# Kernel optimization log

Measured on AMD Instinct MI355X. Metric: run time of the kernel, lower is better.

## Reference

```python
import jax, jax.numpy as jnp
import numpy as np
from jax import lax

STEP_SIZE = 0.1
T0, T1 = 0.0, 1.0
NUM_STEPS = int(abs(T1 - T0) / STEP_SIZE)  # 10 leapfrog steps

B = 65536
N_DIM = 128      # q and p each have N_DIM dims; x has 2*N_DIM
HIDDEN = 512


def setup_inputs() -> dict:
    key = jax.random.key(0)
    k_x, k_w1, k_w2 = jax.random.split(key, 3)
    x = jax.random.normal(k_x, (B, 2 * N_DIM), dtype=jnp.float32)
    # potential MLP: Linear(N_DIM, HIDDEN) -> tanh -> Linear(HIDDEN, 1)
    W1 = jax.random.normal(k_w1, (N_DIM, HIDDEN), dtype=jnp.float32) / np.sqrt(N_DIM)
    b1 = jnp.zeros((HIDDEN,), dtype=jnp.float32)
    W2 = jax.random.normal(k_w2, (HIDDEN, 1), dtype=jnp.float32) / np.sqrt(HIDDEN)
    b2 = jnp.zeros((1,), dtype=jnp.float32)
    return {"x": x, "W1": W1, "b1": b1, "W2": W2, "b2": b2}


def reference(x, W1, b1, W2, b2):
    """Symplectic (leapfrog-style) forward integration of the Hamiltonian ODE.

    H(q,p) = 0.5*sum(p^2) + V(q), V(q) = MLP(q) with scalar output.
    Per step (faithful to the torch loop, grads taken jointly at (q,p)):
        dH/dq = dV/dq,  dH/dp = p
        p <- p - dV/dq * dt
        q <- q + p_old * dt
    """
    dt = jnp.float32(STEP_SIZE)
    n = x.shape[-1] // 2
    q0, p0 = x[..., :n], x[..., n:]

    def V_sum(q):  # sum over batch of scalar potential
        h = jnp.tanh(q @ W1 + b1)          # [B, HIDDEN]
        v = (h @ W2)[..., 0] + b2[0]       # [B]
        return v.sum()

    grad_V = jax.grad(V_sum)  # [B, n] -> dV/dq per sample (sum decouples)

    def step(carry, _):
        q, p = carry
        dH_dq = grad_V(q)      # grads at (q, p_old)
        dH_dp = p
        p_new = p - dH_dq * dt
        q_new = q + dH_dp * dt
        return (q_new, p_new), None

    (qf, pf), _ = lax.scan(step, (q0, p0), None, length=NUM_STEPS)
    return jnp.concatenate([qf, pf], axis=-1)
```

## Files before the change

### kernel.cpp

```cpp
#include <hip/hip_runtime.h>
#include <hip/hip_bf16.h>

typedef float f32x4 __attribute__((ext_vector_type(4)));
typedef __bf16 bf16x8 __attribute__((ext_vector_type(8)));
typedef unsigned short u16x4 __attribute__((ext_vector_type(4)));

#if defined(__has_builtin)
#if __has_builtin(__builtin_amdgcn_exp2f)
#define EXP2F(x) __builtin_amdgcn_exp2f(x)
#else
#define EXP2F(x) exp2f(x)
#endif
#if __has_builtin(__builtin_amdgcn_rcpf)
#define RCPF(x) __builtin_amdgcn_rcpf(x)
#else
#define RCPF(x) (1.0f/(x))
#endif
#else
#define EXP2F(x) exp2f(x)
#define RCPF(x) (1.0f/(x))
#endif

#define MFMA16(a,b,c) __builtin_amdgcn_mfma_f32_16x16x32_bf16((a),(b),(c),0,0,0)

__device__ __forceinline__ unsigned short f2bf(float f) {
  return __builtin_bit_cast(unsigned short, (__bf16)f);
}

__global__ __launch_bounds__(256) void hn_prep(const float* __restrict__ W1,
                                               unsigned short* __restrict__ W1T) {
  int t = blockIdx.x * 256 + threadIdx.x;
  int j = t >> 7, i = t & 127;
  W1T[t] = f2bf(W1[i * 512 + j]);
}

__global__ __launch_bounds__(512, 2) void hn_main(
    const float* __restrict__ x, const float* __restrict__ W1,
    const float* __restrict__ b1, const float* __restrict__ W2,
    const unsigned short* __restrict__ W1T, float* __restrict__ out) {
  __shared__ __align__(16) char w1l[131072];
  __shared__ __align__(16) float b1s[512];
  __shared__ __align__(16) float w2s[512];
  __shared__ __align__(16) char scr[8][2048];

  const int tid = threadIdx.x;
  const int lane = tid & 63;
  const int w = tid >> 6;
  const int m = lane & 15;
  const int g = lane >> 4;

  for (int it = tid; it < 16384; it += 512) {
    int flat = it << 2;
    int i = flat >> 9;
    f32x4 v = *(const f32x4*)(W1 + flat);
    u16x4 pk;
#pragma unroll
    for (int c = 0; c < 4; ++c) pk[c] = f2bf(v[c]);
    int ba = flat << 1;
    *(u16x4*)(w1l + (ba ^ ((i & 7) << 4))) = pk;
  }
  if (tid < 512) { b1s[tid] = b1[tid]; w2s[tid] = W2[tid]; }
  __syncthreads();

  const int b0 = blockIdx.x * 256 + w * 32;

  float q[2][4][8], p[2][4][8];
#pragma unroll
  for (int bf = 0; bf < 2; ++bf)
#pragma unroll
    for (int kb = 0; kb < 4; ++kb) {
      const float* r0 = x + (long)(b0 + m + 16 * bf) * 256 + kb * 32 + g * 8;
      f32x4 a0 = *(const f32x4*)r0;
      f32x4 a1 = *(const f32x4*)(r0 + 4);
      f32x4 c0 = *(const f32x4*)(r0 + 128);
      f32x4 c1 = *(const f32x4*)(r0 + 132);
#pragma unroll
      for (int r = 0; r < 4; ++r) {
        q[bf][kb][r] = a0[r]; q[bf][kb][r + 4] = a1[r];
        p[bf][kb][r] = c0[r]; p[bf][kb][r + 4] = c1[r];
      }
    }

  const char* w1tb = (const char*)W1T;
  char* st = scr[w];

#pragma unroll 1
  for (int step = 0; step < 10; ++step) {
    f32x4 gacc[2][8];
#pragma unroll
    for (int mf = 0; mf < 2; ++mf)
#pragma unroll
      for (int nf = 0; nf < 8; ++nf) gacc[mf][nf] = f32x4{0.f, 0.f, 0.f, 0.f};

#pragma unroll 1
    for (int jblk = 0; jblk < 16; ++jblk) {
      f32x4 z[2][2];
      z[0][0] = f32x4{0.f,0.f,0.f,0.f}; z[0][1] = f32x4{0.f,0.f,0.f,0.f};
      z[1][0] = f32x4{0.f,0.f,0.f,0.f}; z[1][1] = f32x4{0.f,0.f,0.f,0.f};
#pragma unroll
      for (int kb = 0; kb < 4; ++kb) {
        bf16x8 qb0, qb1;
#pragma unroll
        for (int r = 0; r < 8; ++r) {
          qb0[r] = (__bf16)q[0][kb][r];
          qb1[r] = (__bf16)q[1][kb][r];
        }
#pragma unroll
        for (int jf = 0; jf < 2; ++jf) {
          bf16x8 a = *(const bf16x8*)(
              w1tb + (((jblk * 32 + jf * 16 + m) * 128 + kb * 32 + g * 8) << 1));
          z[jf][0] = MFMA16(a, qb0, z[jf][0]);
          z[jf][1] = MFMA16(a, qb1, z[jf][1]);
        }
      }
#pragma unroll
      for (int jf = 0; jf < 2; ++jf) {
        int jb = jblk * 32 + jf * 16 + 4 * g;
        f32x4 b1v = *(const f32x4*)(b1s + jb);
        f32x4 w2v = *(const f32x4*)(w2s + jb);
#pragma unroll
        for (int bf = 0; bf < 2; ++bf) {
          int brow = m + 16 * bf;
          u16x4 pk;
#pragma unroll
          for (int rr = 0; rr < 4; ++rr) {
            float zz = z[jf][bf][rr] + b1v[rr];
            float e = EXP2F(zz * 2.88539008177792681f);
            float th = 1.f - 2.f * RCPF(e + 1.f);
            float s = w2v[rr] * (1.f - th * th);
            pk[rr] = f2bf(s);
          }
          int ba = brow * 64 + (jf * 16 + 4 * g) * 2;
          *(u16x4*)(st + (ba ^ ((brow & 3) << 4))) = pk;
        }
      }
      bf16x8 sA[2];
#pragma unroll
      for (int mf = 0; mf < 2; ++mf) {
        int brow = m + 16 * mf;
        int ba = brow * 64 + g * 16;
        sA[mf] = *(const bf16x8*)(st + (ba ^ ((brow & 3) << 4)));
      }
#pragma unroll
      for (int nf = 0; nf < 8; ++nf) {
        int irow = m + 16 * nf;
        int ba = irow * 1024 + (jblk * 32 + g * 8) * 2;
        bf16x8 bfr = *(const bf16x8*)(w1l + (ba ^ ((irow & 7) << 4)));
        gacc[0][nf] = MFMA16(sA[0], bfr, gacc[0][nf]);
        gacc[1][nf] = MFMA16(sA[1], bfr, gacc[1][nf]);
      }
    }

#pragma unroll
    for (int bf = 0; bf < 2; ++bf)
#pragma unroll
      for (int kb = 0; kb < 4; ++kb)
#pragma unroll
        for (int r = 0; r < 8; ++r)
          q[bf][kb][r] = fmaf(0.1f, p[bf][kb][r], q[bf][kb][r]);

#pragma unroll
    for (int kb = 0; kb < 4; ++kb) {
#pragma unroll
      for (int mf = 0; mf < 2; ++mf)
#pragma unroll
        for (int h = 0; h < 2; ++h) {
          f32x4 gv = gacc[mf][kb * 2 + h];
#pragma unroll
          for (int rr = 0; rr < 4; ++rr) {
            int brow = 4 * g + rr + 16 * mf;
            int ba = brow * 64 + (m + 16 * h) * 2;
            *(unsigned short*)(st + (ba ^ ((brow & 3) << 4))) = f2bf(gv[rr]);
          }
        }
#pragma unroll
      for (int bf = 0; bf < 2; ++bf) {
        int brow = m + 16 * bf;
        int ba = brow * 64 + g * 16;
        bf16x8 gv8 = *(const bf16x8*)(st + (ba ^ ((brow & 3) << 4)));
#pragma unroll
        for (int r = 0; r < 8; ++r)
          p[bf][kb][r] = fmaf(-0.1f, (float)gv8[r], p[bf][kb][r]);
      }
    }
    __syncthreads();
  }

#pragma unroll
  for (int bf = 0; bf < 2; ++bf)
#pragma unroll
    for (int kb = 0; kb < 4; ++kb) {
      float* o = out + (long)(b0 + m + 16 * bf) * 256 + kb * 32 + g * 8;
      f32x4 a0, a1, c0, c1;
#pragma unroll
      for (int r = 0; r < 4; ++r) {
        a0[r] = q[bf][kb][r]; a1[r] = q[bf][kb][r + 4];
        c0[r] = p[bf][kb][r]; c1[r] = p[bf][kb][r + 4];
      }
      *(f32x4*)o = a0; *(f32x4*)(o + 4) = a1;
      *(f32x4*)(o + 128) = c0; *(f32x4*)(o + 132) = c1;
    }
}

extern "C" void kernel_launch(void* const* d_in, const int* in_sizes, int n_in,
                              void* d_out, int out_size, void* d_ws, size_t ws_size,
                              hipStream_t stream) {
  const float* x  = (const float*)d_in[0];
  const float* W1 = (const float*)d_in[1];
  const float* b1 = (const float*)d_in[2];
  const float* W2 = (const float*)d_in[3];
  float* out = (float*)d_out;
  unsigned short* w1t = (unsigned short*)d_ws;

  hipLaunchKernelGGL(hn_prep, dim3(256), dim3(256), 0, stream, W1, w1t);
  hipLaunchKernelGGL(hn_main, dim3(256), dim3(512), 0, stream,
                     x, W1, b1, W2, w1t, out);
}
```

Baseline: 403.2 us.

## Replace LDS scratch transposes with in-register permlane/swizzle exchanges

Removes the per-wave LDS scratch buffer that moved tanh-derivative values and gradients between MFMA output and input layouts. They are now packed to bf16 with v_cvt_pk_bf16_f32 and moved between lanes with v_permlane32_swap and ds_swizzle. The second GEMM swaps its operands so W1 becomes the A operand, and the tanh prescale is folded into b1 with an FMA. This cuts LDS traffic and packing instructions in the inner loop, but relies on the permutation logic exactly matching the MFMA fragment layouts.

```diff
diff --git a/kernel.cpp b/kernel.cpp
--- a/kernel.cpp
+++ b/kernel.cpp
@@ -4,6 +4,8 @@
 typedef float f32x4 __attribute__((ext_vector_type(4)));
 typedef __bf16 bf16x8 __attribute__((ext_vector_type(8)));
 typedef unsigned short u16x4 __attribute__((ext_vector_type(4)));
+typedef unsigned int u32;
+typedef unsigned int u32x4 __attribute__((ext_vector_type(4)));
 
 #if defined(__has_builtin)
 #if __has_builtin(__builtin_amdgcn_exp2f)
@@ -27,6 +29,26 @@
   return __builtin_bit_cast(unsigned short, (__bf16)f);
 }
 
+__device__ __forceinline__ u32 pkbf(float a, float b) {
+  u32 d;
+  asm("v_cvt_pk_bf16_f32 %0, %1, %2" : "=v"(d) : "v"(a), "v"(b));
+  return d;
+}
+
+__device__ __forceinline__ void quad_exch(u32 lo0, u32 hi0, u32 lo1, u32 hi1,
+                                          bool o16, u32 w[4]) {
+  asm("v_permlane32_swap_b32 %0, %1" : "+v"(lo0), "+v"(hi0));
+  asm("v_permlane32_swap_b32 %0, %1" : "+v"(lo1), "+v"(hi1));
+  u32 xlo0 = __builtin_amdgcn_ds_swizzle((int)lo0, 0x401F);
+  u32 xhi0 = __builtin_amdgcn_ds_swizzle((int)hi0, 0x401F);
+  u32 xlo1 = __builtin_amdgcn_ds_swizzle((int)lo1, 0x401F);
+  u32 xhi1 = __builtin_amdgcn_ds_swizzle((int)hi1, 0x401F);
+  w[0] = o16 ? xhi0 : lo0;
+  w[1] = o16 ? xhi1 : lo1;
+  w[2] = o16 ? hi0 : xlo0;
+  w[3] = o16 ? hi1 : xlo1;
+}
+
 __global__ __launch_bounds__(256) void hn_prep(const float* __restrict__ W1,
                                                unsigned short* __restrict__ W1T) {
   int t = blockIdx.x * 256 + threadIdx.x;
@@ -41,13 +63,13 @@
   __shared__ __align__(16) char w1l[131072];
   __shared__ __align__(16) float b1s[512];
   __shared__ __align__(16) float w2s[512];
-  __shared__ __align__(16) char scr[8][2048];
 
   const int tid = threadIdx.x;
   const int lane = tid & 63;
   const int w = tid >> 6;
   const int m = lane & 15;
   const int g = lane >> 4;
+  const bool o16 = (g & 1);
 
   for (int it = tid; it < 16384; it += 512) {
     int flat = it << 2;
@@ -59,7 +81,10 @@
     int ba = flat << 1;
     *(u16x4*)(w1l + (ba ^ ((i & 7) << 4))) = pk;
   }
-  if (tid < 512) { b1s[tid] = b1[tid]; w2s[tid] = W2[tid]; }
+  if (tid < 512) {
+    b1s[tid] = b1[tid] * 2.8853900817779268f;
+    w2s[tid] = W2[tid];
+  }
   __syncthreads();
 
   const int b0 = blockIdx.x * 256 + w * 32;
@@ -81,16 +106,17 @@
       }
     }
 
-  const char* w1tb = (const char*)W1T;
-  char* st = scr[w];
+  const char* aptr = (const char*)W1T + m * 256 + g * 16;
+  const int s45 = (m & 3) << 4, s6 = (m & 4) << 4;
+  const int ybase = ((m * 1024 + g * 16) ^ s45);
 
 #pragma unroll 1
   for (int step = 0; step < 10; ++step) {
     f32x4 gacc[2][8];
 #pragma unroll
-    for (int mf = 0; mf < 2; ++mf)
-#pragma unroll
-      for (int nf = 0; nf < 8; ++nf) gacc[mf][nf] = f32x4{0.f, 0.f, 0.f, 0.f};
+    for (int bf = 0; bf < 2; ++bf)
+#pragma unroll
+      for (int nf = 0; nf < 8; ++nf) gacc[bf][nf] = f32x4{0.f, 0.f, 0.f, 0.f};
 
 #pragma unroll 1
     for (int jblk = 0; jblk < 16; ++jblk) {
@@ -100,54 +126,56 @@
 #pragma unroll
       for (int kb = 0; kb < 4; ++kb) {
         bf16x8 qb0, qb1;
-#pragma unroll
-        for (int r = 0; r < 8; ++r) {
-          qb0[r] = (__bf16)q[0][kb][r];
-          qb1[r] = (__bf16)q[1][kb][r];
+        {
+          u32x4 w0, w1v;
+#pragma unroll
+          for (int h = 0; h < 4; ++h) {
+            w0[h]  = pkbf(q[0][kb][2 * h], q[0][kb][2 * h + 1]);
+            w1v[h] = pkbf(q[1][kb][2 * h], q[1][kb][2 * h + 1]);
+          }
+          qb0 = __builtin_bit_cast(bf16x8, w0);
+          qb1 = __builtin_bit_cast(bf16x8, w1v);
         }
 #pragma unroll
         for (int jf = 0; jf < 2; ++jf) {
-          bf16x8 a = *(const bf16x8*)(
-              w1tb + (((jblk * 32 + jf * 16 + m) * 128 + kb * 32 + g * 8) << 1));
+          bf16x8 a = *(const bf16x8*)(aptr + jblk * 8192 + jf * 4096 + kb * 64);
           z[jf][0] = MFMA16(a, qb0, z[jf][0]);
           z[jf][1] = MFMA16(a, qb1, z[jf][1]);
         }
       }
+      float s4[2][2][4];
 #pragma unroll
       for (int jf = 0; jf < 2; ++jf) {
         int jb = jblk * 32 + jf * 16 + 4 * g;
         f32x4 b1v = *(const f32x4*)(b1s + jb);
         f32x4 w2v = *(const f32x4*)(w2s + jb);
 #pragma unroll
-        for (int bf = 0; bf < 2; ++bf) {
-          int brow = m + 16 * bf;
-          u16x4 pk;
+        for (int bf = 0; bf < 2; ++bf)
 #pragma unroll
           for (int rr = 0; rr < 4; ++rr) {
-            float zz = z[jf][bf][rr] + b1v[rr];
-            float e = EXP2F(zz * 2.88539008177792681f);
-            float th = 1.f - 2.f * RCPF(e + 1.f);
-            float s = w2v[rr] * (1.f - th * th);
-            pk[rr] = f2bf(s);
+            float zz = fmaf(z[jf][bf][rr], 2.8853900817779268f, b1v[rr]);
+            float e = EXP2F(zz);
+            float u = RCPF(e + 1.f);
+            float th = fmaf(-2.f, u, 1.f);
+            s4[jf][bf][rr] = fmaf(-th * th, w2v[rr], w2v[rr]);
           }
-          int ba = brow * 64 + (jf * 16 + 4 * g) * 2;
-          *(u16x4*)(st + (ba ^ ((brow & 3) << 4))) = pk;
-        }
-      }
-      bf16x8 sA[2];
-#pragma unroll
-      for (int mf = 0; mf < 2; ++mf) {
-        int brow = m + 16 * mf;
-        int ba = brow * 64 + g * 16;
-        sA[mf] = *(const bf16x8*)(st + (ba ^ ((brow & 3) << 4)));
-      }
+      }
+      bf16x8 sB[2];
+#pragma unroll
+      for (int bf = 0; bf < 2; ++bf) {
+        u32 Bw[4];
+        quad_exch(pkbf(s4[0][bf][0], s4[0][bf][1]), pkbf(s4[1][bf][0], s4[1][bf][1]),
+                  pkbf(s4[0][bf][2], s4[0][bf][3]), pkbf(s4[1][bf][2], s4[1][bf][3]),
+                  o16, Bw);
+        u32x4 wv; wv[0] = Bw[0]; wv[1] = Bw[1]; wv[2] = Bw[2]; wv[3] = Bw[3];
+        sB[bf] = __builtin_bit_cast(bf16x8, wv);
+      }
+      const int joff = (jblk * 64) ^ s6;
 #pragma unroll
       for (int nf = 0; nf < 8; ++nf) {
-        int irow = m + 16 * nf;
-        int ba = irow * 1024 + (jblk * 32 + g * 8) * 2;
-        bf16x8 bfr = *(const bf16x8*)(w1l + (ba ^ ((irow & 7) << 4)));
-        gacc[0][nf] = MFMA16(sA[0], bfr, gacc[0][nf]);
-        gacc[1][nf] = MFMA16(sA[1], bfr, gacc[1][nf]);
+        bf16x8 af = *(const bf16x8*)(w1l + ybase + nf * 16384 + joff);
+        gacc[0][nf] = MFMA16(af, sB[0], gacc[0][nf]);
+        gacc[1][nf] = MFMA16(af, sB[1], gacc[1][nf]);
       }
     }
 
@@ -160,29 +188,23 @@
           q[bf][kb][r] = fmaf(0.1f, p[bf][kb][r], q[bf][kb][r]);
 
 #pragma unroll
-    for (int kb = 0; kb < 4; ++kb) {
-#pragma unroll
-      for (int mf = 0; mf < 2; ++mf)
-#pragma unroll
-        for (int h = 0; h < 2; ++h) {
-          f32x4 gv = gacc[mf][kb * 2 + h];
-#pragma unroll
-          for (int rr = 0; rr < 4; ++rr) {
-            int brow = 4 * g + rr + 16 * mf;
-            int ba = brow * 64 + (m + 16 * h) * 2;
-            *(unsigned short*)(st + (ba ^ ((brow & 3) << 4))) = f2bf(gv[rr]);
-          }
+    for (int bf = 0; bf < 2; ++bf)
+#pragma unroll
+      for (int kb = 0; kb < 4; ++kb) {
+        u32 Gw[4];
+        quad_exch(pkbf(gacc[bf][2*kb][0],   gacc[bf][2*kb][1]),
+                  pkbf(gacc[bf][2*kb+1][0], gacc[bf][2*kb+1][1]),
+                  pkbf(gacc[bf][2*kb][2],   gacc[bf][2*kb][3]),
+                  pkbf(gacc[bf][2*kb+1][2], gacc[bf][2*kb+1][3]),
+                  o16, Gw);
+#pragma unroll
+        for (int t = 0; t < 4; ++t) {
+          float glo = __builtin_bit_cast(float, Gw[t] << 16);
+          float ghi = __builtin_bit_cast(float, Gw[t] & 0xffff0000u);
+          p[bf][kb][2 * t]     = fmaf(-0.1f, glo, p[bf][kb][2 * t]);
+          p[bf][kb][2 * t + 1] = fmaf(-0.1f, ghi, p[bf][kb][2 * t + 1]);
         }
-#pragma unroll
-      for (int bf = 0; bf < 2; ++bf) {
-        int brow = m + 16 * bf;
-        int ba = brow * 64 + g * 16;
-        bf16x8 gv8 = *(const bf16x8*)(st + (ba ^ ((brow & 3) << 4)));
-#pragma unroll
-        for (int r = 0; r < 8; ++r)
-          p[bf][kb][r] = fmaf(-0.1f, (float)gv8[r], p[bf][kb][r]);
-      }
-    }
+      }
     __syncthreads();
   }
 
```

After: 391.9 us. 2.8% less time.

## Permute W1T and register layouts to drop LDS round-trips for activations and gradients

Applied to the files above, without the earlier changes.

The prep kernel now writes W1T in a permuted row and column order, and q/p are loaded with a matching interleaved per-lane mapping. With that, the tanh-derivative values produced by the first MFMA can feed the second MFMA directly as the B operand, and the gradient accumulator lines up with p's register layout. This removes the per-warp LDS scratch writes and reads for both the activations and the gradient, along with the bf16 rounding of the gradient. It also folds the log2(e) scale into b1 and unrolls the jblk loop by 2, which may raise register pressure.

```diff
diff --git a/kernel.cpp b/kernel.cpp
--- a/kernel.cpp
+++ b/kernel.cpp
@@ -30,7 +30,9 @@
 __global__ __launch_bounds__(256) void hn_prep(const float* __restrict__ W1,
                                                unsigned short* __restrict__ W1T) {
   int t = blockIdx.x * 256 + threadIdx.x;
-  int j = t >> 7, i = t & 127;
+  int rho = t >> 7, io = t & 127;
+  int j = (rho >> 5) * 32 + ((rho >> 2) & 3) * 8 + ((rho >> 4) & 1) * 4 + (rho & 3);
+  int i = (io >> 5) * 32 + ((io & 7) >> 2) * 16 + ((io >> 3) & 3) * 4 + (io & 7 & 3);
   W1T[t] = f2bf(W1[i * 512 + j]);
 }
 
@@ -41,7 +43,6 @@
   __shared__ __align__(16) char w1l[131072];
   __shared__ __align__(16) float b1s[512];
   __shared__ __align__(16) float w2s[512];
-  __shared__ __align__(16) char scr[8][2048];
 
   const int tid = threadIdx.x;
   const int lane = tid & 63;
@@ -59,7 +60,10 @@
     int ba = flat << 1;
     *(u16x4*)(w1l + (ba ^ ((i & 7) << 4))) = pk;
   }
-  if (tid < 512) { b1s[tid] = b1[tid]; w2s[tid] = W2[tid]; }
+  if (tid < 512) {
+    b1s[tid] = b1[tid] * 2.8853900817779268f;
+    w2s[tid] = W2[tid];
+  }
   __syncthreads();
 
   const int b0 = blockIdx.x * 256 + w * 32;
@@ -69,30 +73,32 @@
   for (int bf = 0; bf < 2; ++bf)
 #pragma unroll
     for (int kb = 0; kb < 4; ++kb) {
-      const float* r0 = x + (long)(b0 + m + 16 * bf) * 256 + kb * 32 + g * 8;
-      f32x4 a0 = *(const f32x4*)r0;
-      f32x4 a1 = *(const f32x4*)(r0 + 4);
-      f32x4 c0 = *(const f32x4*)(r0 + 128);
-      f32x4 c1 = *(const f32x4*)(r0 + 132);
-#pragma unroll
-      for (int r = 0; r < 4; ++r) {
-        q[bf][kb][r] = a0[r]; q[bf][kb][r + 4] = a1[r];
-        p[bf][kb][r] = c0[r]; p[bf][kb][r + 4] = c1[r];
+      const float* r0 = x + (long)(b0 + 16 * bf + m) * 256 + kb * 32 + g * 4;
+#pragma unroll
+      for (int h = 0; h < 2; ++h) {
+        f32x4 qv = *(const f32x4*)(r0 + h * 16);
+        f32x4 pv = *(const f32x4*)(r0 + h * 16 + 128);
+#pragma unroll
+        for (int rr = 0; rr < 4; ++rr) {
+          q[bf][kb][4 * h + rr] = qv[rr];
+          p[bf][kb][4 * h + rr] = pv[rr];
+        }
       }
     }
 
-  const char* w1tb = (const char*)W1T;
-  char* st = scr[w];
+  const char* aptr = (const char*)W1T + m * 256 + g * 16;
+  const int s45 = (m & 3) << 4, s6 = (m & 4) << 4;
+  const int ybase = ((m * 1024 + g * 16) ^ s45);
 
 #pragma unroll 1
   for (int step = 0; step < 10; ++step) {
     f32x4 gacc[2][8];
 #pragma unroll
-    for (int mf = 0; mf < 2; ++mf)
-#pragma unroll
-      for (int nf = 0; nf < 8; ++nf) gacc[mf][nf] = f32x4{0.f, 0.f, 0.f, 0.f};
-
-#pragma unroll 1
+    for (int bf = 0; bf < 2; ++bf)
+#pragma unroll
+      for (int nf = 0; nf < 8; ++nf) gacc[bf][nf] = f32x4{0.f, 0.f, 0.f, 0.f};
+
+#pragma unroll 2
     for (int jblk = 0; jblk < 16; ++jblk) {
       f32x4 z[2][2];
       z[0][0] = f32x4{0.f,0.f,0.f,0.f}; z[0][1] = f32x4{0.f,0.f,0.f,0.f};
@@ -107,47 +113,39 @@
         }
 #pragma unroll
         for (int jf = 0; jf < 2; ++jf) {
-          bf16x8 a = *(const bf16x8*)(
-              w1tb + (((jblk * 32 + jf * 16 + m) * 128 + kb * 32 + g * 8) << 1));
+          bf16x8 a = *(const bf16x8*)(aptr + jblk * 8192 + jf * 4096 + kb * 64);
           z[jf][0] = MFMA16(a, qb0, z[jf][0]);
           z[jf][1] = MFMA16(a, qb1, z[jf][1]);
         }
       }
+      float s8[2][8];
 #pragma unroll
       for (int jf = 0; jf < 2; ++jf) {
-        int jb = jblk * 32 + jf * 16 + 4 * g;
-        f32x4 b1v = *(const f32x4*)(b1s + jb);
-        f32x4 w2v = *(const f32x4*)(w2s + jb);
-#pragma unroll
-        for (int bf = 0; bf < 2; ++bf) {
-          int brow = m + 16 * bf;
-          u16x4 pk;
+        f32x4 b1v = *(const f32x4*)(b1s + jblk * 32 + g * 8 + jf * 4);
+        f32x4 w2v = *(const f32x4*)(w2s + jblk * 32 + g * 8 + jf * 4);
+#pragma unroll
+        for (int bf = 0; bf < 2; ++bf)
 #pragma unroll
           for (int rr = 0; rr < 4; ++rr) {
-            float zz = z[jf][bf][rr] + b1v[rr];
-            float e = EXP2F(zz * 2.88539008177792681f);
-            float th = 1.f - 2.f * RCPF(e + 1.f);
-            float s = w2v[rr] * (1.f - th * th);
-            pk[rr] = f2bf(s);
+            float zz = fmaf(z[jf][bf][rr], 2.8853900817779268f, b1v[rr]);
+            float e = EXP2F(zz);
+            float u = RCPF(e + 1.f);
+            float th = fmaf(-2.f, u, 1.f);
+            s8[bf][jf * 4 + rr] = fmaf(-th * th, w2v[rr], w2v[rr]);
           }
-          int ba = brow * 64 + (jf * 16 + 4 * g) * 2;
-          *(u16x4*)(st + (ba ^ ((brow & 3) << 4))) = pk;
-        }
-      }
-      bf16x8 sA[2];
-#pragma unroll
-      for (int mf = 0; mf < 2; ++mf) {
-        int brow = m + 16 * mf;
-        int ba = brow * 64 + g * 16;
-        sA[mf] = *(const bf16x8*)(st + (ba ^ ((brow & 3) << 4)));
-      }
+      }
+      bf16x8 sB0, sB1;
+#pragma unroll
+      for (int r = 0; r < 8; ++r) {
+        sB0[r] = (__bf16)s8[0][r];
+        sB1[r] = (__bf16)s8[1][r];
+      }
+      const int joff = (jblk * 64) ^ s6;
 #pragma unroll
       for (int nf = 0; nf < 8; ++nf) {
-        int irow = m + 16 * nf;
-        int ba = irow * 1024 + (jblk * 32 + g * 8) * 2;
-        bf16x8 bfr = *(const bf16x8*)(w1l + (ba ^ ((irow & 7) << 4)));
-        gacc[0][nf] = MFMA16(sA[0], bfr, gacc[0][nf]);
-        gacc[1][nf] = MFMA16(sA[1], bfr, gacc[1][nf]);
+        bf16x8 af = *(const bf16x8*)(w1l + ybase + nf * 16384 + joff);
+        gacc[0][nf] = MFMA16(af, sB0, gacc[0][nf]);
+        gacc[1][nf] = MFMA16(af, sB1, gacc[1][nf]);
       }
     }
 
@@ -160,29 +158,13 @@
           q[bf][kb][r] = fmaf(0.1f, p[bf][kb][r], q[bf][kb][r]);
 
 #pragma unroll
-    for (int kb = 0; kb < 4; ++kb) {
-#pragma unroll
-      for (int mf = 0; mf < 2; ++mf)
-#pragma unroll
-        for (int h = 0; h < 2; ++h) {
-          f32x4 gv = gacc[mf][kb * 2 + h];
-#pragma unroll
-          for (int rr = 0; rr < 4; ++rr) {
-            int brow = 4 * g + rr + 16 * mf;
-            int ba = brow * 64 + (m + 16 * h) * 2;
-            *(unsigned short*)(st + (ba ^ ((brow & 3) << 4))) = f2bf(gv[rr]);
-          }
-        }
-#pragma unroll
-      for (int bf = 0; bf < 2; ++bf) {
-        int brow = m + 16 * bf;
-        int ba = brow * 64 + g * 16;
-        bf16x8 gv8 = *(const bf16x8*)(st + (ba ^ ((brow & 3) << 4)));
+    for (int bf = 0; bf < 2; ++bf)
+#pragma unroll
+      for (int kb = 0; kb < 4; ++kb)
 #pragma unroll
         for (int r = 0; r < 8; ++r)
-          p[bf][kb][r] = fmaf(-0.1f, (float)gv8[r], p[bf][kb][r]);
-      }
-    }
+          p[bf][kb][r] = fmaf(-0.1f, gacc[bf][2 * kb + (r >> 2)][r & 3], p[bf][kb][r]);
+
     __syncthreads();
   }
 
@@ -190,15 +172,18 @@
   for (int bf = 0; bf < 2; ++bf)
 #pragma unroll
     for (int kb = 0; kb < 4; ++kb) {
-      float* o = out + (long)(b0 + m + 16 * bf) * 256 + kb * 32 + g * 8;
-      f32x4 a0, a1, c0, c1;
-#pragma unroll
-      for (int r = 0; r < 4; ++r) {
-        a0[r] = q[bf][kb][r]; a1[r] = q[bf][kb][r + 4];
-        c0[r] = p[bf][kb][r]; c1[r] = p[bf][kb][r + 4];
-      }
-      *(f32x4*)o = a0; *(f32x4*)(o + 4) = a1;
-      *(f32x4*)(o + 128) = c0; *(f32x4*)(o + 132) = c1;
+      float* o = out + (long)(b0 + 16 * bf + m) * 256 + kb * 32 + g * 4;
+#pragma unroll
+      for (int h = 0; h < 2; ++h) {
+        f32x4 qv, pv;
+#pragma unroll
+        for (int rr = 0; rr < 4; ++rr) {
+          qv[rr] = q[bf][kb][4 * h + rr];
+          pv[rr] = p[bf][kb][4 * h + rr];
+        }
+        *(f32x4*)(o + h * 16) = qv;
+        *(f32x4*)(o + h * 16 + 128) = pv;
+      }
     }
 }
 
```

Result: faster. 345.0 us (-14.4%).
